# Performance work log

Hardware: AMD Instinct MI355X
Metric: run time of the kernel (lower is better)

Reference implementation:

```python
import jax, jax.numpy as jnp
import numpy as np

D = 4096
B_BITS = 4
NUM_CENTROIDS = 2 ** B_BITS  # 16 uniform centroids in [-1, 1]
N_TOKENS = 8192


def setup_inputs() -> dict:
    key = jax.random.key(0)
    kx, kp = jax.random.split(key)
    x = jax.random.normal(kx, (N_TOKENS, D), dtype=jnp.float32)
    # Orthogonal rotation Pi via QR of a random Gaussian (matches torch.linalg.qr)
    rand_mat = jax.random.normal(kp, (D, D), dtype=jnp.float32)
    Pi, _ = jnp.linalg.qr(rand_mat)
    centroids = jnp.linspace(-1.0, 1.0, NUM_CENTROIDS, dtype=jnp.float32)
    return {"x": x, "Pi": Pi, "centroids": centroids}


def _quantize(y, centroids):
    # Centroids are uniformly spaced on [-1, 1]; nearest-centroid argmin has the
    # closed form below (identical result to the broadcast |y - c| argmin, without
    # materializing the O(N*d*2^b) distance tensor).
    n = centroids.shape[0]
    scale = (n - 1) * 0.5
    idx = jnp.clip(jnp.round((y + 1.0) * scale), 0, n - 1).astype(jnp.int32)
    return centroids[idx]


def reference(x, Pi, centroids):
    y = x @ Pi.T                      # [N, d] rotate into quantization basis
    y_q = _quantize(y, centroids)     # nearest uniform centroid
    x_tilde = y_q @ Pi                # rotate back
    return x_tilde
```

## Files before the change

### kernel.cpp

```cpp
#include <hip/hip_runtime.h>
#include <hip/hip_bf16.h>

#define DD 4096
#define NTOK 8192

using u16 = unsigned short;

typedef __attribute__((ext_vector_type(8))) short bfrag;
typedef __attribute__((ext_vector_type(4))) float ffrag;
typedef __attribute__((ext_vector_type(4))) float f32x4v;

__device__ __forceinline__ u16 f2bf(float f) {
  unsigned u = __float_as_uint(f);
  u += 0x7FFFu + ((u >> 16) & 1u);
  return (u16)(u >> 16);
}
__device__ __forceinline__ float bf2f(u16 u) {
  return __uint_as_float(((unsigned)u) << 16);
}

#define GLDS16(g, l)                                                  \
  __builtin_amdgcn_global_load_lds(                                   \
      (__attribute__((address_space(1))) const void*)(g),             \
      (__attribute__((address_space(3))) void*)(l), 16, 0, 0)

#define MEMFENCE() asm volatile("" ::: "memory")

__global__ void __launch_bounds__(256) split_bf16_kernel(
    const float* __restrict__ in, u16* __restrict__ hi,
    u16* __restrict__ lo, long n4) {
  long i = (long)blockIdx.x * blockDim.x + threadIdx.x;
  const long stride = (long)gridDim.x * blockDim.x;
  for (; i < n4; i += stride) {
    f32x4v v = reinterpret_cast<const f32x4v*>(in)[i];
    u16 h[4], l[4];
#pragma unroll
    for (int j = 0; j < 4; ++j) {
      float f = v[j];
      u16 hb = f2bf(f);
      h[j] = hb;
      l[j] = f2bf(f - bf2f(hb));
    }
    ushort4 hv, lv;
    hv.x = h[0]; hv.y = h[1]; hv.z = h[2]; hv.w = h[3];
    lv.x = l[0]; lv.y = l[1]; lv.z = l[2]; lv.w = l[3];
    reinterpret_cast<ushort4*>(hi)[i] = hv;
    reinterpret_cast<ushort4*>(lo)[i] = lv;
  }
}

__global__ void __launch_bounds__(256) transpose_bf16_kernel(
    const float* __restrict__ in, u16* __restrict__ out, int R, int C) {
  __shared__ u16 tile[64][65];
  const int bc = blockIdx.x << 6;
  const int br = blockIdx.y << 6;
  const int tc = threadIdx.x & 63;
  const int tr0 = threadIdx.x >> 6;
#pragma unroll
  for (int p = 0; p < 16; ++p) {
    int r = tr0 + (p << 2);
    tile[tc][r] = f2bf(in[(size_t)(br + r) * C + (bc + tc)]);
  }
  __syncthreads();
#pragma unroll
  for (int p = 0; p < 16; ++p) {
    int orow = tr0 + (p << 2);
    out[(size_t)(bc + orow) * R + (br + tc)] = tile[orow][tc];
  }
}

template <int NSEG, bool QUANT>
__global__ void __launch_bounds__(512, 2) gemm256_kernel(
    const u16* __restrict__ A0, const u16* __restrict__ A1,
    const u16* __restrict__ B0, const u16* __restrict__ B1,
    void* __restrict__ Cout, const float* __restrict__ cent,
    int M, int N) {
  constexpr int NT = NSEG * 64;
  __shared__ __align__(16) char SM[131072];
  __shared__ float clut[16];
  const int tid = threadIdx.x;
  if (QUANT && tid < 16) clut[tid] = cent[tid];

  const int nbn = N >> 8;
  const int nwg = (M >> 8) * nbn;
  int wg = blockIdx.x;
  wg = (wg & 7) * (nwg >> 3) + (wg >> 3);
  const int tm = (wg / nbn) << 8;
  const int tn = (wg % nbn) << 8;

  const int lane = tid & 63;
  const int wv = tid >> 6;
  const int wm = wv >> 2;
  const int wn = wv & 3;
  const int l15 = lane & 15;
  const int kslc = lane >> 4;
  const int cXor = (lane & 7) << 4;

  const size_t thrOff =
      (size_t)(wv * 8 + (lane >> 3)) * 4096 + 8 * ((lane & 7) ^ (lane >> 3));
  const int ldsThr = wv * 1024 + lane * 16;

  auto STAGE = [&](int kind, int tau) {
    if (tau >= NT) return;
    const int b = tau & 1;
    const int seg = (NSEG == 3) ? (tau >> 6) : 0;
    const size_t ktE = (size_t)(tau & 63) * 64;
    const u16* src;
    char* lds;
    if (kind >= 2) {
      const u16* bbase = (NSEG == 3 && seg == 2) ? B1 : B0;
      const int idx = kind - 2;
      src = bbase + (size_t)(tn + idx * 128) * 4096 + ktE + thrOff;
      lds = SM + b * 65536 + 32768 + idx * 16384 + ldsThr;
    } else {
      const u16* abase = (NSEG == 3 && seg == 1) ? A1 : A0;
      src = abase + (size_t)(tm + kind * 128) * 4096 + ktE + thrOff;
      lds = SM + b * 65536 + kind * 16384 + ldsThr;
    }
    GLDS16(src, lds);
    GLDS16(src + 262144, lds + 8192);
  };

#define LDSA(b, f, s)                                                      \
  (*reinterpret_cast<const bfrag*>(                                        \
      SM + (b) * 65536 + wm * 16384 + (((f) * 16 + l15) << 7) +            \
      ((((s) << 6) | (kslc << 4)) ^ cXor)))
#define LDSB(b, f, s)                                                      \
  (*reinterpret_cast<const bfrag*>(                                        \
      SM + (b) * 65536 + 32768 + (wn >> 1) * 16384 +                       \
      ((((wn & 1) * 64) + (f) * 16 + l15) << 7) +                          \
      ((((s) << 6) | (kslc << 4)) ^ cXor)))

  ffrag acc[8][4];
#pragma unroll
  for (int m = 0; m < 8; ++m)
#pragma unroll
    for (int n = 0; n < 4; ++n) acc[m][n] = {0.f, 0.f, 0.f, 0.f};

  STAGE(0, 0); STAGE(1, 0); STAGE(2, 0); STAGE(3, 0);
  STAGE(2, 1); STAGE(3, 1);
  asm volatile("s_waitcnt vmcnt(4)" ::: "memory");
  MEMFENCE();
  __builtin_amdgcn_s_barrier();

  bfrag Af[4], Bf[4];

  for (int t = 0; t < NT; ++t) {
    const int b = t & 1;
#pragma unroll
    for (int p = 0; p < 4; ++p) {
      const int s = p >> 1;
      const int mb = (p & 1) * 4;
      if ((p & 1) == 0) {
#pragma unroll
        for (int n = 0; n < 4; ++n) Bf[n] = LDSB(b, n, s);
      }
#pragma unroll
      for (int m = 0; m < 4; ++m) Af[m] = LDSA(b, mb + m, s);
      if (p == 0) STAGE(0, t + 1);
      else if (p == 1) STAGE(1, t + 1);
      else if (p == 3) { STAGE(2, t + 2); STAGE(3, t + 2); }
      MEMFENCE();
      __builtin_amdgcn_s_barrier();
      asm volatile("s_waitcnt lgkmcnt(0)" ::: "memory");
      __builtin_amdgcn_s_setprio(1);
#pragma unroll
      for (int m = 0; m < 4; ++m)
#pragma unroll
        for (int n = 0; n < 4; ++n)
          acc[mb + m][n] = __builtin_amdgcn_mfma_f32_16x16x32_bf16(
              Af[m], Bf[n], acc[mb + m][n], 0, 0, 0);
      __builtin_amdgcn_s_setprio(0);
      if (p == 3) {
        if (t == NT - 2)
          asm volatile("s_waitcnt vmcnt(0)" ::: "memory");
        else if (t < NT - 2)
          asm volatile("s_waitcnt vmcnt(4)" ::: "memory");
      }
      MEMFENCE();
      __builtin_amdgcn_s_barrier();
    }
  }

  const int r0 = tm + wm * 128 + kslc * 4;
  const int c0 = tn + wn * 64 + l15;
  if constexpr (QUANT) {
    u16* Y = reinterpret_cast<u16*>(Cout);
#pragma unroll
    for (int m = 0; m < 8; ++m)
#pragma unroll
      for (int n = 0; n < 4; ++n)
#pragma unroll
        for (int r = 0; r < 4; ++r) {
          float y = acc[m][n][r];
          float s = rintf((y + 1.0f) * 7.5f);
          int idx = (int)s;
          idx = idx < 0 ? 0 : (idx > 15 ? 15 : idx);
          Y[(size_t)(r0 + m * 16 + r) * N + (c0 + n * 16)] = f2bf(clut[idx]);
        }
  } else {
    float* Co = reinterpret_cast<float*>(Cout);
#pragma unroll
    for (int m = 0; m < 8; ++m)
#pragma unroll
      for (int n = 0; n < 4; ++n)
#pragma unroll
        for (int r = 0; r < 4; ++r)
          Co[(size_t)(r0 + m * 16 + r) * N + (c0 + n * 16)] = acc[m][n][r];
  }
#undef LDSA
#undef LDSB
}

extern "C" void kernel_launch(void* const* d_in, const int* in_sizes, int n_in,
                              void* d_out, int out_size, void* d_ws, size_t ws_size,
                              hipStream_t stream) {
  const float* x = (const float*)d_in[0];
  const float* Pi = (const float*)d_in[1];
  const float* cent = (const float*)d_in[2];
  float* out = (float*)d_out;

  const size_t MB = (size_t)1 << 20;
  if (ws_size < 288 * MB) return;

  char* ws = (char*)d_ws;
  u16* x_hi = (u16*)(ws + 0 * MB);
  u16* x_lo = (u16*)(ws + 64 * MB);
  u16* p_hi = (u16*)(ws + 128 * MB);
  u16* p_lo = (u16*)(ws + 160 * MB);
  u16* piT  = (u16*)(ws + 192 * MB);
  u16* yq   = (u16*)(ws + 224 * MB);

  split_bf16_kernel<<<2048, 256, 0, stream>>>(x, x_hi, x_lo, (long)NTOK * DD / 4);
  split_bf16_kernel<<<1024, 256, 0, stream>>>(Pi, p_hi, p_lo, (long)DD * DD / 4);
  transpose_bf16_kernel<<<dim3(DD / 64, DD / 64), 256, 0, stream>>>(Pi, piT, DD, DD);

  const int nwg = (NTOK / 256) * (DD / 256);
  gemm256_kernel<3, true><<<nwg, 512, 0, stream>>>(
      x_hi, x_lo, p_hi, p_lo, yq, cent, NTOK, DD);
  gemm256_kernel<1, false><<<nwg, 512, 0, stream>>>(
      yq, nullptr, piT, nullptr, out, nullptr, NTOK, DD);
}
```

Baseline: 1.150 ms.

## Ping-pong register fragments to overlap LDS reads with MFMA in GEMM loop

Restructures the GEMM main loop to double-buffer A/B register fragments (even and odd sets). Each phase now prefetches the next phase's LDS fragments, including the first fragments of the next k-tile, while the current 16 MFMAs run. This removes the explicit lgkmcnt(0) stall before every MFMA block. It costs extra VGPRs for the second fragment set, and the global-load wait changes from vmcnt(4) to vmcnt(0) with the B-tile prefetch moved later, which may expose more memory latency.

```diff
diff --git a/kernel.cpp b/kernel.cpp
--- a/kernel.cpp
+++ b/kernel.cpp
@@ -131,55 +131,73 @@
       ((((wn & 1) * 64) + (f) * 16 + l15) << 7) +                          \
       ((((s) << 6) | (kslc << 4)) ^ cXor)))
 
+#define MFMA16(Aset, Bset, mb)                                             \
+  __builtin_amdgcn_s_setprio(1);                                           \
+  _Pragma("unroll")                                                        \
+  for (int m = 0; m < 4; ++m)                                              \
+    _Pragma("unroll")                                                      \
+    for (int n = 0; n < 4; ++n)                                            \
+      acc[(mb) + m][n] = __builtin_amdgcn_mfma_f32_16x16x32_bf16(          \
+          Aset[m], Bset[n], acc[(mb) + m][n], 0, 0, 0);                    \
+  __builtin_amdgcn_s_setprio(0);
+
   ffrag acc[8][4];
 #pragma unroll
   for (int m = 0; m < 8; ++m)
 #pragma unroll
     for (int n = 0; n < 4; ++n) acc[m][n] = {0.f, 0.f, 0.f, 0.f};
+
+  bfrag AfE[4], AfO[4], BfE[4], BfO[4];
 
   STAGE(0, 0); STAGE(1, 0); STAGE(2, 0); STAGE(3, 0);
   STAGE(2, 1); STAGE(3, 1);
   asm volatile("s_waitcnt vmcnt(4)" ::: "memory");
   MEMFENCE();
   __builtin_amdgcn_s_barrier();
-
-  bfrag Af[4], Bf[4];
+#pragma unroll
+  for (int m = 0; m < 4; ++m) AfE[m] = LDSA(0, m, 0);
+#pragma unroll
+  for (int n = 0; n < 4; ++n) BfE[n] = LDSB(0, n, 0);
 
   for (int t = 0; t < NT; ++t) {
     const int b = t & 1;
 #pragma unroll
-    for (int p = 0; p < 4; ++p) {
-      const int s = p >> 1;
-      const int mb = (p & 1) * 4;
-      if ((p & 1) == 0) {
-#pragma unroll
-        for (int n = 0; n < 4; ++n) Bf[n] = LDSB(b, n, s);
-      }
-#pragma unroll
-      for (int m = 0; m < 4; ++m) Af[m] = LDSA(b, mb + m, s);
-      if (p == 0) STAGE(0, t + 1);
-      else if (p == 1) STAGE(1, t + 1);
-      else if (p == 3) { STAGE(2, t + 2); STAGE(3, t + 2); }
-      MEMFENCE();
-      __builtin_amdgcn_s_barrier();
-      asm volatile("s_waitcnt lgkmcnt(0)" ::: "memory");
-      __builtin_amdgcn_s_setprio(1);
-#pragma unroll
-      for (int m = 0; m < 4; ++m)
-#pragma unroll
-        for (int n = 0; n < 4; ++n)
-          acc[mb + m][n] = __builtin_amdgcn_mfma_f32_16x16x32_bf16(
-              Af[m], Bf[n], acc[mb + m][n], 0, 0, 0);
-      __builtin_amdgcn_s_setprio(0);
-      if (p == 3) {
-        if (t == NT - 2)
-          asm volatile("s_waitcnt vmcnt(0)" ::: "memory");
-        else if (t < NT - 2)
-          asm volatile("s_waitcnt vmcnt(4)" ::: "memory");
-      }
-      MEMFENCE();
-      __builtin_amdgcn_s_barrier();
+    for (int m = 0; m < 4; ++m) AfO[m] = LDSA(b, 4 + m, 0);
+    STAGE(0, t + 1); STAGE(1, t + 1);
+    MEMFENCE();
+    __builtin_amdgcn_s_barrier();
+    MFMA16(AfE, BfE, 0)
+    MEMFENCE();
+    __builtin_amdgcn_s_barrier();
+#pragma unroll
+    for (int m = 0; m < 4; ++m) AfE[m] = LDSA(b, m, 1);
+#pragma unroll
+    for (int n = 0; n < 4; ++n) BfO[n] = LDSB(b, n, 1);
+    MEMFENCE();
+    __builtin_amdgcn_s_barrier();
+    MFMA16(AfO, BfE, 4)
+    MEMFENCE();
+    __builtin_amdgcn_s_barrier();
+#pragma unroll
+    for (int m = 0; m < 4; ++m) AfO[m] = LDSA(b, 4 + m, 1);
+    MEMFENCE();
+    __builtin_amdgcn_s_barrier();
+    MFMA16(AfE, BfO, 0)
+    asm volatile("s_waitcnt vmcnt(0)" ::: "memory");
+    MEMFENCE();
+    __builtin_amdgcn_s_barrier();
+    if (t + 1 < NT) {
+#pragma unroll
+      for (int m = 0; m < 4; ++m) AfE[m] = LDSA(b ^ 1, m, 0);
+#pragma unroll
+      for (int n = 0; n < 4; ++n) BfE[n] = LDSB(b ^ 1, n, 0);
     }
+    STAGE(2, t + 2); STAGE(3, t + 2);
+    MEMFENCE();
+    __builtin_amdgcn_s_barrier();
+    MFMA16(AfO, BfO, 4)
+    MEMFENCE();
+    __builtin_amdgcn_s_barrier();
   }
 
   const int r0 = tm + wm * 128 + kslc * 4;
@@ -210,6 +228,7 @@
   }
 #undef LDSA
 #undef LDSB
+#undef MFMA16
 }
 
 extern "C" void kernel_launch(void* const* d_in, const int* in_sizes, int n_in,
```

New measurement: 1.097 ms. 1.05x faster.

## Fuse three split-bf16 GEMM passes into one K-loop sharing operand tiles

Applied to the files above, without the earlier changes.

The first GEMM used to stream K three times (hi·hi, lo·hi, hi·lo), reloading the A and B tiles for each pass. It is replaced by a kernel that stages the A_hi, A_lo, B_hi and B_lo tiles for each 32-wide K slice together and issues all three MFMA products from them. This removes the redundant global-to-LDS traffic for the shared hi operands. It also adds a new LDS swizzle layout. In exchange there are more barriers per iteration, a full vmcnt(0) wait every step and a shallower prefetch, which may expose memory latency. The second GEMM is simply de-templated.

```diff
diff --git a/kernel.cpp b/kernel.cpp
--- a/kernel.cpp
+++ b/kernel.cpp
@@ -69,17 +69,149 @@
   }
 }
 
-template <int NSEG, bool QUANT>
-__global__ void __launch_bounds__(512, 2) gemm256_kernel(
-    const u16* __restrict__ A0, const u16* __restrict__ A1,
-    const u16* __restrict__ B0, const u16* __restrict__ B1,
-    void* __restrict__ Cout, const float* __restrict__ cent,
-    int M, int N) {
-  constexpr int NT = NSEG * 64;
+__global__ void __launch_bounds__(512, 2) gemm_fused3_kernel(
+    const u16* __restrict__ Ah_, const u16* __restrict__ Al_,
+    const u16* __restrict__ Bh_, const u16* __restrict__ Bl_,
+    u16* __restrict__ Yq, const float* __restrict__ cent, int M, int N) {
   __shared__ __align__(16) char SM[131072];
   __shared__ float clut[16];
   const int tid = threadIdx.x;
-  if (QUANT && tid < 16) clut[tid] = cent[tid];
+  if (tid < 16) clut[tid] = cent[tid];
+
+  const int nbn = N >> 8;
+  const int nwg = (M >> 8) * nbn;
+  int wg = blockIdx.x;
+  wg = (wg & 7) * (nwg >> 3) + (wg >> 3);
+  const int tm = (wg / nbn) << 8;
+  const int tn = (wg % nbn) << 8;
+
+  const int lane = tid & 63;
+  const int wv = tid >> 6;
+  const int wm = wv >> 2;
+  const int wn = wv & 3;
+  const int l15 = lane & 15;
+  const int kslc = lane >> 4;
+
+  const int Dst = tid * 16;
+  const int Lg = Dst ^ (((Dst >> 7) & 7) << 4);
+  const int srow = Lg >> 6;
+  const int scol = (Lg & 63) >> 1;
+  const size_t sOffA = (size_t)(tm + srow) * 4096 + scol;
+  const size_t sOffB = (size_t)(tn + srow) * 4096 + scol;
+
+  auto STAGE = [&](int u, const u16* base, int tau) {
+    if (tau >= 128) return;
+    const u16* src = base + (u < 2 ? sOffA : sOffB) + tau * 32;
+    char* lds = SM + (tau & 1) * 65536 + u * 16384 + Dst;
+    GLDS16(src, lds);
+    GLDS16(src + (size_t)128 * 4096, lds + 8192);
+  };
+
+  const int slot16 = ((((l15 & 1) << 2) | kslc) ^ (l15 >> 1)) << 4;
+  const int aOff = wm * 8192 + (l15 >> 1) * 128 + slot16;
+  const int bOff = wn * 4096 + (l15 >> 1) * 128 + slot16;
+
+#define LDSF(b, ubase, off, f)                                           \
+  (*reinterpret_cast<const bfrag*>(SM + (b) * 65536 + (ubase) + (off) +  \
+                                   (f) * 1024))
+
+  ffrag acc[8][4];
+#pragma unroll
+  for (int m = 0; m < 8; ++m)
+#pragma unroll
+    for (int n = 0; n < 4; ++n) acc[m][n] = {0.f, 0.f, 0.f, 0.f};
+
+  bfrag Ahf[8], Alf[4], Bhf[4], Blf[4];
+
+  STAGE(0, Ah_, 0); STAGE(1, Al_, 0); STAGE(2, Bh_, 0); STAGE(3, Bl_, 0);
+  asm volatile("s_waitcnt vmcnt(0)" ::: "memory");
+  MEMFENCE();
+  __builtin_amdgcn_s_barrier();
+
+#define MFMA16(Aset, a0, Bset, mb)                                       \
+  __builtin_amdgcn_s_setprio(1);                                         \
+  _Pragma("unroll")                                                      \
+  for (int m = 0; m < 4; ++m)                                            \
+    _Pragma("unroll")                                                    \
+    for (int n = 0; n < 4; ++n)                                          \
+      acc[(mb) + m][n] = __builtin_amdgcn_mfma_f32_16x16x32_bf16(        \
+          Aset[(a0) + m], Bset[n], acc[(mb) + m][n], 0, 0, 0);           \
+  __builtin_amdgcn_s_setprio(0);
+
+  for (int t = 0; t < 128; ++t) {
+    const int b = t & 1;
+#pragma unroll
+    for (int f = 0; f < 4; ++f) Ahf[f] = LDSF(b, 0, aOff, f);
+#pragma unroll
+    for (int f = 0; f < 4; ++f) Bhf[f] = LDSF(b, 32768, bOff, f);
+    STAGE(0, Ah_, t + 1); STAGE(1, Al_, t + 1);
+    MEMFENCE();
+    __builtin_amdgcn_s_barrier();
+    asm volatile("s_waitcnt lgkmcnt(0)" ::: "memory");
+    MFMA16(Ahf, 0, Bhf, 0)
+    MEMFENCE();
+    __builtin_amdgcn_s_barrier();
+#pragma unroll
+    for (int f = 0; f < 4; ++f) Ahf[4 + f] = LDSF(b, 0, aOff, 4 + f);
+    STAGE(2, Bh_, t + 1); STAGE(3, Bl_, t + 1);
+    MEMFENCE();
+    __builtin_amdgcn_s_barrier();
+    asm volatile("s_waitcnt lgkmcnt(0)" ::: "memory");
+    MFMA16(Ahf, 4, Bhf, 4)
+    MEMFENCE();
+    __builtin_amdgcn_s_barrier();
+#pragma unroll
+    for (int f = 0; f < 4; ++f) Alf[f] = LDSF(b, 16384, aOff, f);
+    MEMFENCE();
+    __builtin_amdgcn_s_barrier();
+    asm volatile("s_waitcnt lgkmcnt(0)" ::: "memory");
+    MFMA16(Alf, 0, Bhf, 0)
+    MEMFENCE();
+    __builtin_amdgcn_s_barrier();
+#pragma unroll
+    for (int f = 0; f < 4; ++f) Alf[f] = LDSF(b, 16384, aOff, 4 + f);
+    MEMFENCE();
+    __builtin_amdgcn_s_barrier();
+    asm volatile("s_waitcnt lgkmcnt(0)" ::: "memory");
+    MFMA16(Alf, 0, Bhf, 4)
+    MEMFENCE();
+    __builtin_amdgcn_s_barrier();
+#pragma unroll
+    for (int f = 0; f < 4; ++f) Blf[f] = LDSF(b, 49152, bOff, f);
+    MEMFENCE();
+    __builtin_amdgcn_s_barrier();
+    asm volatile("s_waitcnt lgkmcnt(0)" ::: "memory");
+    MFMA16(Ahf, 0, Blf, 0)
+    MFMA16(Ahf, 4, Blf, 4)
+    asm volatile("s_waitcnt vmcnt(0)" ::: "memory");
+    MEMFENCE();
+    __builtin_amdgcn_s_barrier();
+  }
+
+  const int r0 = tm + wm * 128 + kslc * 4;
+  const int c0 = tn + wn * 64 + l15;
+#pragma unroll
+  for (int m = 0; m < 8; ++m)
+#pragma unroll
+    for (int n = 0; n < 4; ++n)
+#pragma unroll
+      for (int r = 0; r < 4; ++r) {
+        float y = acc[m][n][r];
+        float s = rintf((y + 1.0f) * 7.5f);
+        int idx = (int)s;
+        idx = idx < 0 ? 0 : (idx > 15 ? 15 : idx);
+        Yq[(size_t)(r0 + m * 16 + r) * N + (c0 + n * 16)] = f2bf(clut[idx]);
+      }
+#undef LDSF
+#undef MFMA16
+}
+
+__global__ void __launch_bounds__(512, 2) gemm256_bt_kernel(
+    const u16* __restrict__ A0, const u16* __restrict__ B0,
+    float* __restrict__ Cout, int M, int N) {
+  constexpr int NT = 64;
+  __shared__ __align__(16) char SM[131072];
+  const int tid = threadIdx.x;
 
   const int nbn = N >> 8;
   const int nwg = (M >> 8) * nbn;
@@ -103,18 +235,15 @@
   auto STAGE = [&](int kind, int tau) {
     if (tau >= NT) return;
     const int b = tau & 1;
-    const int seg = (NSEG == 3) ? (tau >> 6) : 0;
-    const size_t ktE = (size_t)(tau & 63) * 64;
+    const size_t ktE = (size_t)tau * 64;
     const u16* src;
     char* lds;
     if (kind >= 2) {
-      const u16* bbase = (NSEG == 3 && seg == 2) ? B1 : B0;
       const int idx = kind - 2;
-      src = bbase + (size_t)(tn + idx * 128) * 4096 + ktE + thrOff;
+      src = B0 + (size_t)(tn + idx * 128) * 4096 + ktE + thrOff;
       lds = SM + b * 65536 + 32768 + idx * 16384 + ldsThr;
     } else {
-      const u16* abase = (NSEG == 3 && seg == 1) ? A1 : A0;
-      src = abase + (size_t)(tm + kind * 128) * 4096 + ktE + thrOff;
+      src = A0 + (size_t)(tm + kind * 128) * 4096 + ktE + thrOff;
       lds = SM + b * 65536 + kind * 16384 + ldsThr;
     }
     GLDS16(src, lds);
@@ -184,30 +313,13 @@
 
   const int r0 = tm + wm * 128 + kslc * 4;
   const int c0 = tn + wn * 64 + l15;
-  if constexpr (QUANT) {
-    u16* Y = reinterpret_cast<u16*>(Cout);
-#pragma unroll
-    for (int m = 0; m < 8; ++m)
-#pragma unroll
-      for (int n = 0; n < 4; ++n)
-#pragma unroll
-        for (int r = 0; r < 4; ++r) {
-          float y = acc[m][n][r];
-          float s = rintf((y + 1.0f) * 7.5f);
-          int idx = (int)s;
-          idx = idx < 0 ? 0 : (idx > 15 ? 15 : idx);
-          Y[(size_t)(r0 + m * 16 + r) * N + (c0 + n * 16)] = f2bf(clut[idx]);
-        }
-  } else {
-    float* Co = reinterpret_cast<float*>(Cout);
-#pragma unroll
-    for (int m = 0; m < 8; ++m)
-#pragma unroll
-      for (int n = 0; n < 4; ++n)
-#pragma unroll
-        for (int r = 0; r < 4; ++r)
-          Co[(size_t)(r0 + m * 16 + r) * N + (c0 + n * 16)] = acc[m][n][r];
-  }
+#pragma unroll
+  for (int m = 0; m < 8; ++m)
+#pragma unroll
+    for (int n = 0; n < 4; ++n)
+#pragma unroll
+      for (int r = 0; r < 4; ++r)
+        Cout[(size_t)(r0 + m * 16 + r) * N + (c0 + n * 16)] = acc[m][n][r];
 #undef LDSA
 #undef LDSB
 }
@@ -235,9 +347,7 @@
   split_bf16_kernel<<<1024, 256, 0, stream>>>(Pi, p_hi, p_lo, (long)DD * DD / 4);
   transpose_bf16_kernel<<<dim3(DD / 64, DD / 64), 256, 0, stream>>>(Pi, piT, DD, DD);
 
-  const int nwg = (NTOK / 256) * (DD / 256);
-  gemm256_kernel<3, true><<<nwg, 512, 0, stream>>>(
+  gemm_fused3_kernel<<<512, 512, 0, stream>>>(
       x_hi, x_lo, p_hi, p_lo, yq, cent, NTOK, DD);
-  gemm256_kernel<1, false><<<nwg, 512, 0, stream>>>(
-      yq, nullptr, piT, nullptr, out, nullptr, NTOK, DD);
-}
+  gemm256_bt_kernel<<<512, 512, 0, stream>>>(yq, piT, out, NTOK, DD);
+}
```

New measurement: 1.023 ms. 11.0% less time.
